# Kernel optimization log

Measured on AMD Instinct MI355X. Metric: run time of the kernel, lower is better.

Reference implementation:

```python
import jax, jax.numpy as jnp
import numpy as np

EPS = 1e-12  # torch F.normalize eps
NEG_INF = -1000000000.0


def _l2_normalize(a, axis):
    norm = jnp.sqrt(jnp.sum(a * a, axis=axis, keepdims=True))
    return a / jnp.maximum(norm, EPS)


def setup_inputs() -> dict:
    key = jax.random.key(0)
    k1, k2, k3 = jax.random.split(key, 3)
    B, D, M, C = 1024, 512, 60000, 10
    x = jax.random.normal(k1, (B, D), dtype=jnp.float32)
    keys = jax.random.normal(k2, (M, D), dtype=jnp.float32)
    values = jax.random.randint(k3, (M,), 0, C, dtype=jnp.int64)
    return {"x": x, "keys": keys, "values": values, "k": 50, "num_classes": C}


def reference(x, keys, values, k, num_classes):
    # query -> normalize -> cosine sim -> mask empty -> topk -> soft vote
    x_n = _l2_normalize(x, axis=1)          # [B, D]
    k_n = _l2_normalize(keys, axis=1)       # [M, D]
    scores = jnp.einsum('bd,md->bm', x_n, k_n)  # [B, M]
    empty = (values == -1)                  # [M]
    scores = jnp.where(empty[None, :], NEG_INF, scores)
    top_scores, top_idx = jax.lax.top_k(scores, k)   # [B, k]
    top_labels = values[top_idx]            # [B, k]
    valid = top_labels != -1
    safe_lbl = jnp.where(valid, top_labels, 0)
    safe_score = jnp.where(valid, top_scores, 0.0)
    B = x.shape[0]
    logits = jnp.zeros((B, num_classes), dtype=scores.dtype)
    logits = logits.at[jnp.arange(B)[:, None], safe_lbl].add(safe_score)
    return logits
```

## Files before the change

### kernel.cpp

```cpp
#include <hip/hip_runtime.h>
#include <math.h>

#define BM 128
#define BN 128
#define EPSV 1e-12f
#define NEG_INF_V -1000000000.0f
#define NBINS 2048
#define FBINS 1024
#define FSCALE 5120.0f
#define SCAP 2048
#define CAP 2048
#define SSCAP 1024
#define TAU 0.10f

typedef __attribute__((ext_vector_type(8))) short bf16x8;
typedef __attribute__((ext_vector_type(4))) float f32x4;

__device__ __forceinline__ unsigned short f2bf(float f) {
    unsigned int u = __float_as_uint(f);
    unsigned int r = (u + 0x7fffu + ((u >> 16) & 1u)) >> 16;
    return (unsigned short)r;
}
__device__ __forceinline__ float bf2f(unsigned short h) {
    return __uint_as_float(((unsigned int)h) << 16);
}
__device__ __forceinline__ void split3(float v, unsigned short& h0,
                                       unsigned short& h1, unsigned short& h2) {
    h0 = f2bf(v); float r = v - bf2f(h0);
    h1 = f2bf(r); r -= bf2f(h1);
    h2 = f2bf(r);
}
__device__ __forceinline__ void gload_lds16(const unsigned short* g, const unsigned short* l) {
    __builtin_amdgcn_global_load_lds((const __attribute__((address_space(1))) void*)g,
                                     (__attribute__((address_space(3))) void*)l, 16, 0, 0);
}

__global__ void xnsplit_kernel(const float* __restrict__ x, float* __restrict__ xn,
                               unsigned short* __restrict__ Xs, size_t xplane, int D) {
    int row = blockIdx.x;
    int lane = threadIdx.x;
    const float4* xr = (const float4*)(x + (size_t)row * D);
    float4* xo = (float4*)(xn + (size_t)row * D);
    int per = (D / 4) / 64;
    float ss = 0.f;
    float4 v[2];
    for (int i = 0; i < per; ++i) {
        float4 t = xr[lane * per + i];
        v[i] = t;
        ss += t.x * t.x + t.y * t.y + t.z * t.z + t.w * t.w;
    }
    for (int off = 32; off >= 1; off >>= 1) ss += __shfl_xor(ss, off);
    float denom = fmaxf(sqrtf(ss), EPSV);
    float vals[8];
    for (int i = 0; i < per; ++i) {
        float4 t = v[i];
        t.x /= denom; t.y /= denom; t.z /= denom; t.w /= denom;
        xo[lane * per + i] = t;
        vals[i * 4 + 0] = t.x; vals[i * 4 + 1] = t.y;
        vals[i * 4 + 2] = t.z; vals[i * 4 + 3] = t.w;
    }
    unsigned short h0[8], h1[8], h2[8];
#pragma unroll
    for (int i = 0; i < 8; ++i) split3(vals[i], h0[i], h1[i], h2[i]);
    size_t off0 = (size_t)row * D + lane * 8;
    *(bf16x8*)(Xs + off0)              = *(bf16x8*)h0;
    *(bf16x8*)(Xs + xplane + off0)     = *(bf16x8*)h1;
    *(bf16x8*)(Xs + 2 * xplane + off0) = *(bf16x8*)h2;
}

__global__ void kinv_kernel(const float* __restrict__ keys, float* __restrict__ kinv,
                            int M, int D) {
    int wave = threadIdx.x >> 6;
    int lane = threadIdx.x & 63;
    int row = blockIdx.x * 4 + wave;
    if (row >= M) return;
    const float4* kr = (const float4*)(keys + (size_t)row * D);
    int per = (D / 4) / 64;
    float ss = 0.f;
    for (int i = 0; i < per; ++i) {
        float4 t = kr[lane * per + i];
        ss += t.x * t.x + t.y * t.y + t.z * t.z + t.w * t.w;
    }
    for (int off = 32; off >= 1; off >>= 1) ss += __shfl_xor(ss, off);
    if (lane == 0) kinv[row] = 1.0f / fmaxf(sqrtf(ss), EPSV);
}

__global__ __launch_bounds__(256)
void ksplit_kernel(const float* __restrict__ keys, const float* __restrict__ kinv,
                   unsigned short* __restrict__ K0, unsigned short* __restrict__ K1,
                   unsigned short* __restrict__ K2, int M, int D, int nk) {
    const int ct = blockIdx.x / nk;
    const int t  = blockIdx.x % nk;
    const size_t blk = (size_t)blockIdx.x * 4096;
#pragma unroll
    for (int half = 0; half < 2; ++half) {
        int sig = half * 256 + threadIdx.x;
        int tau = sig >> 6;
        int mp  = (sig >> 2) & 15;
        int qp  = sig & 3;
        int row = ct * 128 + tau * 16 + mp;
        int qs  = qp ^ (mp & 3);
        unsigned short h0[8], h1[8], h2[8];
        if (row < M) {
            float inv = kinv[row];
            const float* src = keys + (size_t)row * D + t * 32 + qs * 8;
#pragma unroll
            for (int i = 0; i < 8; ++i) split3(src[i] * inv, h0[i], h1[i], h2[i]);
        } else {
#pragma unroll
            for (int i = 0; i < 8; ++i) { h0[i] = 0; h1[i] = 0; h2[i] = 0; }
        }
        size_t off = blk + (size_t)sig * 8;
        *(bf16x8*)(K0 + off) = *(bf16x8*)h0;
        *(bf16x8*)(K1 + off) = *(bf16x8*)h1;
        *(bf16x8*)(K2 + off) = *(bf16x8*)h2;
    }
}

__global__ __launch_bounds__(256, 3)
void gemm_kernel(const unsigned short* __restrict__ Xs,
                 const unsigned short* __restrict__ Kp,
                 const int* __restrict__ values,
                 int2* __restrict__ cand, int* __restrict__ cnt,
                 int M, int D, int nk, int nct, size_t xplane, size_t kplane) {
    const int l  = blockIdx.x;
    const int ct = (l & 7) + ((l >> 6) << 3);
    const int rt = (l >> 3) & 7;
    if (ct >= nct) return;

    __shared__ unsigned short Bs[2][3 * 4096];

    const int tid  = threadIdx.x;
    const int lane = tid & 63;
    const int w    = tid >> 6;
    const int wx   = w >> 1, wy = w & 1;
    const int row0 = rt * BM, col0 = ct * BN;
    const int mq   = lane & 15;
    const int qd   = lane >> 4;
    const int bswz = mq * 32 + ((qd ^ (mq & 3)) << 3);

    f32x4 acc[4][4];
#pragma unroll
    for (int i = 0; i < 4; ++i)
#pragma unroll
        for (int j = 0; j < 4; ++j) acc[i][j] = (f32x4){0.f, 0.f, 0.f, 0.f};

#define STAGE(t_, buf_)                                                          \
    {                                                                            \
        const size_t blk_ = ((size_t)ct * nk + (t_)) * 4096;                     \
        _Pragma("unroll")                                                        \
        for (int i_ = 0; i_ < 6; ++i_) {                                         \
            int s_ = w + i_ * 4;                                                 \
            int sp_ = s_ >> 3, pt_ = s_ & 7;                                     \
            gload_lds16(Kp + (size_t)sp_ * kplane + blk_ + pt_ * 512 + lane * 8, \
                        &Bs[buf_][sp_ * 4096 + pt_ * 512]);                      \
        }                                                                        \
    }

    STAGE(0, 0);

    const unsigned short* arow_base = Xs + (size_t)(row0 + wx * 64 + mq) * D + qd * 8;

    for (int t = 0; t < nk; ++t) {
        const int buf = t & 1;
        __syncthreads();

        bf16x8 af[3][4];
#pragma unroll
        for (int s = 0; s < 3; ++s)
#pragma unroll
            for (int ta = 0; ta < 4; ++ta)
                af[s][ta] = *(const bf16x8*)(arow_base + (size_t)s * xplane +
                                             (size_t)ta * 16 * D + t * 32);

        if (t + 1 < nk) STAGE(t + 1, buf ^ 1);

#pragma unroll
        for (int sb = 0; sb < 3; ++sb) {
            bf16x8 bfr[4];
#pragma unroll
            for (int tb = 0; tb < 4; ++tb)
                bfr[tb] = *(const bf16x8*)&Bs[buf][sb * 4096 + (wy * 4 + tb) * 512 + bswz];
#pragma unroll
            for (int sa = 0; sa <= 2 - sb; ++sa) {
#pragma unroll
                for (int ta = 0; ta < 4; ++ta)
#pragma unroll
                    for (int tb = 0; tb < 4; ++tb)
                        acc[ta][tb] = __builtin_amdgcn_mfma_f32_16x16x32_bf16(
                            af[sa][ta], bfr[tb], acc[ta][tb], 0, 0, 0);
            }
        }
    }

    int ncol[4]; bool okn[4];
#pragma unroll
    for (int tb = 0; tb < 4; ++tb) {
        int n = col0 + wy * 64 + tb * 16 + mq;
        ncol[tb] = n;
        okn[tb] = (n < M) && (values[n] != -1);
    }
#pragma unroll
    for (int ta = 0; ta < 4; ++ta) {
        int rbase = row0 + wx * 64 + ta * 16 + qd * 4;
#pragma unroll
        for (int tb = 0; tb < 4; ++tb) {
            if (!okn[tb]) continue;
#pragma unroll
            for (int rg = 0; rg < 4; ++rg) {
                float s = acc[ta][tb][rg];
                if (s >= TAU) {
                    int r = rbase + rg;
                    int pos = atomicAdd(&cnt[r], 1);
                    if (pos < CAP) cand[(size_t)r * CAP + pos] =
                        make_int2(__float_as_int(s), ncol[tb]);
                }
            }
        }
    }
#undef STAGE
}

__device__ __forceinline__ int fbin(float s) {
    return (int)fminf((s - TAU) * FSCALE, (float)(FBINS - 1));
}
__device__ __forceinline__ int score_bin(float s) {
    float t = fminf(fmaxf((s + 1.0f) * 1024.0f, 0.0f), 2047.0f);
    return (int)t;
}

__global__ __launch_bounds__(256)
void select_kernel(const float* __restrict__ xn, const float* __restrict__ keys,
                   const float* __restrict__ kinv, const int* __restrict__ values,
                   const int* __restrict__ kptr, float* __restrict__ out,
                   const int2* __restrict__ cand, const int* __restrict__ cnt,
                   int M, int D, int C) {
    const int row = blockIdx.x;
    const int tid = threadIdx.x;
    const int K = *kptr;

    __shared__ float cs[SCAP];
    __shared__ int ci[SCAP];
    __shared__ int hist[NBINS];
    __shared__ float ss[SSCAP];
    __shared__ int si[SSCAP];
    __shared__ float xrow[512];
    __shared__ float accs[32];
    __shared__ int scnt, mcnt, tb;

    const int n0 = cnt[row];
    bool fast = (n0 >= K && n0 <= CAP);
    int m = 0;

    if (tid < 32) accs[tid] = 0.f;
    if (tid == 0) { scnt = 0; mcnt = 0; }

    if (fast) {
        for (int i = tid; i < FBINS; i += 256) hist[i] = 0;
        __syncthreads();
        for (int i = tid; i < n0; i += 256) {
            int2 p = cand[(size_t)row * CAP + i];
            float s = __int_as_float(p.x);
            cs[i] = s; ci[i] = p.y;
            atomicAdd(&hist[fbin(s)], 1);
        }
        __syncthreads();
        if (tid < 64) {
            const int lane = tid;
            int csum = 0;
#pragma unroll
            for (int j = 0; j < FBINS / 64; ++j) csum += hist[lane * (FBINS / 64) + j];
            int sfx = csum;
#pragma unroll
            for (int off = 1; off < 64; off <<= 1) {
                int o = __shfl_down(sfx, off);
                if (lane + off < 64) sfx += o;
            }
            unsigned long long mask = __ballot(sfx >= K);
            int L = 63 - __builtin_clzll(mask);
            int above = (L == 63) ? 0 : __shfl(sfx, L + 1);
            if (lane == L) {
                int c = above;
                int t = L * (FBINS / 64);
                for (int j = FBINS / 64 - 1; j >= 0; --j) {
                    c += hist[L * (FBINS / 64) + j];
                    if (c >= K) { t = L * (FBINS / 64) + j; break; }
                }
                tb = t;
            }
        }
        __syncthreads();
        const int T = tb;
        for (int i = tid; i < n0; i += 256) {
            if (fbin(cs[i]) >= T) {
                int p = atomicAdd(&mcnt, 1);
                if (p < SSCAP) { ss[p] = cs[i]; si[p] = ci[i]; }
            }
        }
        __syncthreads();
        m = mcnt;
        if (m > SSCAP) fast = false;
    }

    if (!fast) {
        for (int d = tid; d < D; d += 256) xrow[d] = xn[(size_t)row * D + d];
        for (int i = tid; i < NBINS; i += 256) hist[i] = 0;
        __syncthreads();
        for (int mm = tid; mm < M; mm += 256) {
            float s;
            if (values[mm] == -1) s = NEG_INF_V;
            else {
                const float4* kr = (const float4*)(keys + (size_t)mm * D);
                float sum = 0.f;
                for (int d4 = 0; d4 < D / 4; ++d4) {
                    float4 t = kr[d4];
                    const float4* xq = (const float4*)&xrow[d4 * 4];
                    sum += t.x * xq->x + t.y * xq->y + t.z * xq->z + t.w * xq->w;
                }
                s = sum * kinv[mm];
            }
            atomicAdd(&hist[score_bin(s)], 1);
        }
        __syncthreads();
        if (tid < 64) {
            const int lane = tid;
            int csum = 0;
#pragma unroll
            for (int j = 0; j < NBINS / 64; ++j) csum += hist[lane * (NBINS / 64) + j];
            int sfx = csum;
#pragma unroll
            for (int off = 1; off < 64; off <<= 1) {
                int o = __shfl_down(sfx, off);
                if (lane + off < 64) sfx += o;
            }
            unsigned long long mask = __ballot(sfx >= K);
            int L = 63 - __builtin_clzll(mask);
            int above = (L == 63) ? 0 : __shfl(sfx, L + 1);
            if (lane == L) {
                int c = above;
                int t = L * (NBINS / 64);
                for (int j = NBINS / 64 - 1; j >= 0; --j) {
                    c += hist[L * (NBINS / 64) + j];
                    if (c >= K) { t = L * (NBINS / 64) + j; break; }
                }
                tb = t;
            }
        }
        __syncthreads();
        const int T = tb;
        for (int mm = tid; mm < M; mm += 256) {
            float s;
            if (values[mm] == -1) s = NEG_INF_V;
            else {
                const float4* kr = (const float4*)(keys + (size_t)mm * D);
                float sum = 0.f;
                for (int d4 = 0; d4 < D / 4; ++d4) {
                    float4 t = kr[d4];
                    const float4* xq = (const float4*)&xrow[d4 * 4];
                    sum += t.x * xq->x + t.y * xq->y + t.z * xq->z + t.w * xq->w;
                }
                s = sum * kinv[mm];
            }
            if (score_bin(s) >= T) {
                int p = atomicAdd(&scnt, 1);
                if (p < SCAP) { cs[p] = s; ci[p] = mm; }
            }
        }
        __syncthreads();
        m = scnt < SCAP ? scnt : SCAP;
    }

    const float* rs = fast ? ss : cs;
    const int* ri = fast ? si : ci;
    for (int i = tid; i < m; i += 256) {
        float s = rs[i];
        int idx = ri[i];
        int rank = 0;
        for (int j = 0; j < m; ++j) {
            float sj = rs[j];
            rank += (sj > s) || (sj == s && ri[j] < idx);
        }
        if (rank < K) {
            int lbl = values[idx];
            if (lbl >= 0) atomicAdd(&accs[lbl], s);
        }
    }
    __syncthreads();
    if (tid < C) out[(size_t)row * C + tid] = accs[tid];
}

extern "C" void kernel_launch(void* const* d_in, const int* in_sizes, int n_in,
                              void* d_out, int out_size, void* d_ws, size_t ws_size,
                              hipStream_t stream) {
    const float* x = (const float*)d_in[0];
    const float* keys = (const float*)d_in[1];
    const int* values = (const int*)d_in[2];
    const int* kptr = (const int*)d_in[3];
    float* out = (float*)d_out;

    const int M = in_sizes[2];
    const int D = in_sizes[1] / M;
    const int B = in_sizes[0] / D;
    const int C = out_size / B;
    const int nk = D / 32;
    const int nct = (M + BN - 1) / BN;
    const size_t xplane = (size_t)B * D;
    const size_t kplane = (size_t)nct * nk * 4096;

    char* wp = (char*)d_ws;
    float* xn = (float*)wp;                wp += (size_t)B * D * 4;
    float* kinv = (float*)wp;              wp += ((size_t)M * 4 + 255) / 256 * 256;
    int* cnt = (int*)wp;                   wp += (size_t)B * 4;
    int2* cand = (int2*)wp;                wp += (size_t)B * CAP * 8;
    unsigned short* Xs = (unsigned short*)wp;  wp += 3 * xplane * 2;
    unsigned short* K0 = (unsigned short*)wp;  wp += kplane * 2;
    unsigned short* K1 = (unsigned short*)wp;  wp += kplane * 2;
    unsigned short* K2 = (unsigned short*)wp;

    hipMemsetAsync(cnt, 0, (size_t)B * sizeof(int), stream);

    xnsplit_kernel<<<B, 64, 0, stream>>>(x, xn, Xs, xplane, D);
    kinv_kernel<<<(M + 3) / 4, 256, 0, stream>>>(keys, kinv, M, D);
    ksplit_kernel<<<nct * nk, 256, 0, stream>>>(keys, kinv, K0, K1, K2, M, D, nk);

    int ngrid = 64 * ((nct + 7) / 8);
    gemm_kernel<<<ngrid, 256, 0, stream>>>(Xs, K0, values, cand, cnt,
                                           M, D, nk, nct, xplane, kplane);

    select_kernel<<<B, 256, 0, stream>>>(xn, keys, kinv, values, kptr, out,
                                         cand, cnt, M, D, C);
}
```

Before: 733.7 us.

## Replace bf16x3 split GEMM with scaled fp16x2 split and fuse key normalization

```diff
diff --git a/kernel.cpp b/kernel.cpp
--- a/kernel.cpp
+++ b/kernel.cpp
@@ -13,22 +13,15 @@
 #define SSCAP 1024
 #define TAU 0.10f
 
-typedef __attribute__((ext_vector_type(8))) short bf16x8;
+typedef __attribute__((ext_vector_type(8))) _Float16 f16x8;
 typedef __attribute__((ext_vector_type(4))) float f32x4;
 
-__device__ __forceinline__ unsigned short f2bf(float f) {
-    unsigned int u = __float_as_uint(f);
-    unsigned int r = (u + 0x7fffu + ((u >> 16) & 1u)) >> 16;
-    return (unsigned short)r;
-}
-__device__ __forceinline__ float bf2f(unsigned short h) {
-    return __uint_as_float(((unsigned int)h) << 16);
-}
-__device__ __forceinline__ void split3(float v, unsigned short& h0,
-                                       unsigned short& h1, unsigned short& h2) {
-    h0 = f2bf(v); float r = v - bf2f(h0);
-    h1 = f2bf(r); r -= bf2f(h1);
-    h2 = f2bf(r);
+union hpack { _Float16 h[8]; f16x8 v; };
+
+__device__ __forceinline__ void split2(float v, _Float16& h0, _Float16& h1) {
+    float sv = v * 64.0f;
+    h0 = (_Float16)sv;
+    h1 = (_Float16)((sv - (float)h0) * 2048.0f);
 }
 __device__ __forceinline__ void gload_lds16(const unsigned short* g, const unsigned short* l) {
     __builtin_amdgcn_global_load_lds((const __attribute__((address_space(1))) void*)g,
@@ -59,65 +52,72 @@
         vals[i * 4 + 0] = t.x; vals[i * 4 + 1] = t.y;
         vals[i * 4 + 2] = t.z; vals[i * 4 + 3] = t.w;
     }
-    unsigned short h0[8], h1[8], h2[8];
-#pragma unroll
-    for (int i = 0; i < 8; ++i) split3(vals[i], h0[i], h1[i], h2[i]);
+    hpack p0, p1;
+#pragma unroll
+    for (int i = 0; i < 8; ++i) split2(vals[i], p0.h[i], p1.h[i]);
     size_t off0 = (size_t)row * D + lane * 8;
-    *(bf16x8*)(Xs + off0)              = *(bf16x8*)h0;
-    *(bf16x8*)(Xs + xplane + off0)     = *(bf16x8*)h1;
-    *(bf16x8*)(Xs + 2 * xplane + off0) = *(bf16x8*)h2;
-}
-
-__global__ void kinv_kernel(const float* __restrict__ keys, float* __restrict__ kinv,
-                            int M, int D) {
-    int wave = threadIdx.x >> 6;
-    int lane = threadIdx.x & 63;
-    int row = blockIdx.x * 4 + wave;
-    if (row >= M) return;
-    const float4* kr = (const float4*)(keys + (size_t)row * D);
-    int per = (D / 4) / 64;
-    float ss = 0.f;
-    for (int i = 0; i < per; ++i) {
-        float4 t = kr[lane * per + i];
-        ss += t.x * t.x + t.y * t.y + t.z * t.z + t.w * t.w;
-    }
-    for (int off = 32; off >= 1; off >>= 1) ss += __shfl_xor(ss, off);
-    if (lane == 0) kinv[row] = 1.0f / fmaxf(sqrtf(ss), EPSV);
+    *(f16x8*)(Xs + off0)          = p0.v;
+    *(f16x8*)(Xs + xplane + off0) = p1.v;
 }
 
 __global__ __launch_bounds__(256)
-void ksplit_kernel(const float* __restrict__ keys, const float* __restrict__ kinv,
-                   unsigned short* __restrict__ K0, unsigned short* __restrict__ K1,
-                   unsigned short* __restrict__ K2, int M, int D, int nk) {
-    const int ct = blockIdx.x / nk;
-    const int t  = blockIdx.x % nk;
-    const size_t blk = (size_t)blockIdx.x * 4096;
-#pragma unroll
-    for (int half = 0; half < 2; ++half) {
-        int sig = half * 256 + threadIdx.x;
-        int tau = sig >> 6;
-        int mp  = (sig >> 2) & 15;
-        int qp  = sig & 3;
-        int row = ct * 128 + tau * 16 + mp;
-        int qs  = qp ^ (mp & 3);
-        unsigned short h0[8], h1[8], h2[8];
-        if (row < M) {
-            float inv = kinv[row];
-            const float* src = keys + (size_t)row * D + t * 32 + qs * 8;
-#pragma unroll
-            for (int i = 0; i < 8; ++i) split3(src[i] * inv, h0[i], h1[i], h2[i]);
-        } else {
-#pragma unroll
-            for (int i = 0; i < 8; ++i) { h0[i] = 0; h1[i] = 0; h2[i] = 0; }
-        }
-        size_t off = blk + (size_t)sig * 8;
-        *(bf16x8*)(K0 + off) = *(bf16x8*)h0;
-        *(bf16x8*)(K1 + off) = *(bf16x8*)h1;
-        *(bf16x8*)(K2 + off) = *(bf16x8*)h2;
-    }
-}
-
-__global__ __launch_bounds__(256, 3)
+void kinvsplit_kernel(const float* __restrict__ keys, float* __restrict__ kinv,
+                      unsigned short* __restrict__ K0, unsigned short* __restrict__ K1,
+                      int M, int D, int nk) {
+    const int ct = blockIdx.x;
+    const int tid = threadIdx.x;
+    const int w = tid >> 6, lane = tid & 63;
+    __shared__ float linv[128];
+
+    for (int i = 0; i < 32; ++i) {
+        int rl = w * 32 + i;
+        int row = ct * 128 + rl;
+        if (row >= M) break;
+        const float4* kr = (const float4*)(keys + (size_t)row * D);
+        float ssum = 0.f;
+        int per = (D / 4) / 64;
+        for (int p = 0; p < per; ++p) {
+            float4 t = kr[lane * per + p];
+            ssum += t.x * t.x + t.y * t.y + t.z * t.z + t.w * t.w;
+        }
+        for (int off = 32; off >= 1; off >>= 1) ssum += __shfl_xor(ssum, off);
+        if (lane == 0) {
+            float inv = 1.0f / fmaxf(sqrtf(ssum), EPSV);
+            linv[rl] = inv;
+            kinv[row] = inv;
+        }
+    }
+    __syncthreads();
+
+    for (int t = 0; t < nk; ++t) {
+        const size_t blk = ((size_t)ct * nk + t) * 4096;
+#pragma unroll
+        for (int half = 0; half < 2; ++half) {
+            int sig = half * 256 + tid;
+            int tau = sig >> 6;
+            int mp  = (sig >> 2) & 15;
+            int qp  = sig & 3;
+            int rl  = tau * 16 + mp;
+            int row = ct * 128 + rl;
+            int qs  = qp ^ (mp & 3);
+            hpack p0, p1;
+            if (row < M) {
+                float inv = linv[rl];
+                const float* src = keys + (size_t)row * D + t * 32 + qs * 8;
+#pragma unroll
+                for (int i = 0; i < 8; ++i) split2(src[i] * inv, p0.h[i], p1.h[i]);
+            } else {
+#pragma unroll
+                for (int i = 0; i < 8; ++i) { p0.h[i] = (_Float16)0.f; p1.h[i] = (_Float16)0.f; }
+            }
+            size_t off = blk + (size_t)sig * 8;
+            *(f16x8*)(K0 + off) = p0.v;
+            *(f16x8*)(K1 + off) = p1.v;
+        }
+    }
+}
+
+__global__ __launch_bounds__(256, 2)
 void gemm_kernel(const unsigned short* __restrict__ Xs,
                  const unsigned short* __restrict__ Kp,
                  const int* __restrict__ values,
@@ -128,7 +128,7 @@
     const int rt = (l >> 3) & 7;
     if (ct >= nct) return;
 
-    __shared__ unsigned short Bs[2][3 * 4096];
+    __shared__ unsigned short Bs[2][2 * 4096];
 
     const int tid  = threadIdx.x;
     const int lane = tid & 63;
@@ -139,17 +139,20 @@
     const int qd   = lane >> 4;
     const int bswz = mq * 32 + ((qd ^ (mq & 3)) << 3);
 
-    f32x4 acc[4][4];
+    f32x4 P0[4][4], P1[4][4];
 #pragma unroll
     for (int i = 0; i < 4; ++i)
 #pragma unroll
-        for (int j = 0; j < 4; ++j) acc[i][j] = (f32x4){0.f, 0.f, 0.f, 0.f};
+        for (int j = 0; j < 4; ++j) {
+            P0[i][j] = (f32x4){0.f, 0.f, 0.f, 0.f};
+            P1[i][j] = (f32x4){0.f, 0.f, 0.f, 0.f};
+        }
 
 #define STAGE(t_, buf_)                                                          \
     {                                                                            \
         const size_t blk_ = ((size_t)ct * nk + (t_)) * 4096;                     \
         _Pragma("unroll")                                                        \
-        for (int i_ = 0; i_ < 6; ++i_) {                                         \
+        for (int i_ = 0; i_ < 4; ++i_) {                                         \
             int s_ = w + i_ * 4;                                                 \
             int sp_ = s_ >> 3, pt_ = s_ & 7;                                     \
             gload_lds16(Kp + (size_t)sp_ * kplane + blk_ + pt_ * 512 + lane * 8, \
@@ -165,31 +168,45 @@
         const int buf = t & 1;
         __syncthreads();
 
-        bf16x8 af[3][4];
-#pragma unroll
-        for (int s = 0; s < 3; ++s)
+        f16x8 af0[4], af1[4];
+#pragma unroll
+        for (int ta = 0; ta < 4; ++ta)
+            af0[ta] = *(const f16x8*)(arow_base + (size_t)ta * 16 * D + t * 32);
+#pragma unroll
+        for (int ta = 0; ta < 4; ++ta)
+            af1[ta] = *(const f16x8*)(arow_base + xplane + (size_t)ta * 16 * D + t * 32);
+
+        if (t + 1 < nk) STAGE(t + 1, buf ^ 1);
+
+        {
+            f16x8 b1[4];
+#pragma unroll
+            for (int tb = 0; tb < 4; ++tb)
+                b1[tb] = *(const f16x8*)&Bs[buf][4096 + (wy * 4 + tb) * 512 + bswz];
 #pragma unroll
             for (int ta = 0; ta < 4; ++ta)
-                af[s][ta] = *(const bf16x8*)(arow_base + (size_t)s * xplane +
-                                             (size_t)ta * 16 * D + t * 32);
-
-        if (t + 1 < nk) STAGE(t + 1, buf ^ 1);
-
-#pragma unroll
-        for (int sb = 0; sb < 3; ++sb) {
-            bf16x8 bfr[4];
+#pragma unroll
+                for (int tb = 0; tb < 4; ++tb)
+                    P1[ta][tb] = __builtin_amdgcn_mfma_f32_16x16x32_f16(
+                        af0[ta], b1[tb], P1[ta][tb], 0, 0, 0);
+        }
+        {
+            f16x8 b0[4];
 #pragma unroll
             for (int tb = 0; tb < 4; ++tb)
-                bfr[tb] = *(const bf16x8*)&Bs[buf][sb * 4096 + (wy * 4 + tb) * 512 + bswz];
-#pragma unroll
-            for (int sa = 0; sa <= 2 - sb; ++sa) {
-#pragma unroll
-                for (int ta = 0; ta < 4; ++ta)
-#pragma unroll
-                    for (int tb = 0; tb < 4; ++tb)
-                        acc[ta][tb] = __builtin_amdgcn_mfma_f32_16x16x32_bf16(
-                            af[sa][ta], bfr[tb], acc[ta][tb], 0, 0, 0);
-            }
+                b0[tb] = *(const f16x8*)&Bs[buf][(wy * 4 + tb) * 512 + bswz];
+#pragma unroll
+            for (int ta = 0; ta < 4; ++ta)
+#pragma unroll
+                for (int tb = 0; tb < 4; ++tb)
+                    P0[ta][tb] = __builtin_amdgcn_mfma_f32_16x16x32_f16(
+                        af0[ta], b0[tb], P0[ta][tb], 0, 0, 0);
+#pragma unroll
+            for (int ta = 0; ta < 4; ++ta)
+#pragma unroll
+                for (int tb = 0; tb < 4; ++tb)
+                    P1[ta][tb] = __builtin_amdgcn_mfma_f32_16x16x32_f16(
+                        af1[ta], b0[tb], P1[ta][tb], 0, 0, 0);
         }
     }
 
@@ -208,7 +225,7 @@
             if (!okn[tb]) continue;
 #pragma unroll
             for (int rg = 0; rg < 4; ++rg) {
-                float s = acc[ta][tb][rg];
+                float s = (P0[ta][tb][rg] + P1[ta][tb][rg] * 4.8828125e-4f) * 2.44140625e-4f;
                 if (s >= TAU) {
                     int r = rbase + rg;
                     int pos = atomicAdd(&cnt[r], 1);
@@ -412,16 +429,14 @@
     float* kinv = (float*)wp;              wp += ((size_t)M * 4 + 255) / 256 * 256;
     int* cnt = (int*)wp;                   wp += (size_t)B * 4;
     int2* cand = (int2*)wp;                wp += (size_t)B * CAP * 8;
-    unsigned short* Xs = (unsigned short*)wp;  wp += 3 * xplane * 2;
+    unsigned short* Xs = (unsigned short*)wp;  wp += 2 * xplane * 2;
     unsigned short* K0 = (unsigned short*)wp;  wp += kplane * 2;
-    unsigned short* K1 = (unsigned short*)wp;  wp += kplane * 2;
-    unsigned short* K2 = (unsigned short*)wp;
+    unsigned short* K1 = (unsigned short*)wp;
 
     hipMemsetAsync(cnt, 0, (size_t)B * sizeof(int), stream);
 
     xnsplit_kernel<<<B, 64, 0, stream>>>(x, xn, Xs, xplane, D);
-    kinv_kernel<<<(M + 3) / 4, 256, 0, stream>>>(keys, kinv, M, D);
-    ksplit_kernel<<<nct * nk, 256, 0, stream>>>(keys, kinv, K0, K1, K2, M, D, nk);
+    kinvsplit_kernel<<<nct, 256, 0, stream>>>(keys, kinv, K0, K1, M, D, nk);
 
     int ngrid = 64 * ((nct + 7) / 8);
     gemm_kernel<<<ngrid, 256, 0, stream>>>(Xs, K0, values, cand, cnt,
```

Result: faster. 675.5 us (-7.9%).
